# Kernel optimization log

Measured on AMD Instinct MI355X. Metric: run time of the kernel, lower is better.

Reference implementation:

```python
import jax, jax.numpy as jnp
import numpy as np

THRESH = 0.5
MARGIN = 0.1
SCALE_POS = 2.0
SCALE_NEG = 40.0
EPSILON = 1e-5


def setup_inputs() -> dict:
    key = jax.random.key(0)
    kx, kl = jax.random.split(key)
    B, D, N_CLASSES = 4096, 1024, 256
    x = jax.random.normal(kx, (B, D), dtype=jnp.float32)
    # L2-normalize embeddings (standard for multi-similarity loss; keeps sim in [-1, 1])
    x = x / jnp.linalg.norm(x, axis=1, keepdims=True)
    labels = jax.random.randint(kl, (B,), 0, N_CLASSES, dtype=jnp.int64)
    return {"x": x, "labels": labels}


def reference(x, labels):
    B = x.shape[0]
    sim = jnp.matmul(x, x.T)  # [B, B]

    eye = jnp.eye(B, dtype=bool)
    same = labels[:, None] == labels[None, :]
    pos_mask = same & ~eye                      # positives excl. self
    neg_mask = ~same                            # negatives
    pos_valid = pos_mask & (sim < 1.0 - EPSILON)  # pos_pair_ after < 1-eps filter

    # per-row hardest stats (inf/-inf where empty)
    min_pos = jnp.min(jnp.where(pos_valid, sim, jnp.inf), axis=1)   # min over pos_pair_
    max_neg = jnp.max(jnp.where(neg_mask, sim, -jnp.inf), axis=1)   # max over neg_pair_

    # mined pairs
    neg_keep = neg_mask & (sim + MARGIN > min_pos[:, None])
    pos_keep = pos_valid & (sim - MARGIN < max_neg[:, None])

    has_row = (pos_valid.any(axis=1) & neg_mask.any(axis=1)
               & pos_keep.any(axis=1) & neg_keep.any(axis=1))

    pos_sum = jnp.sum(jnp.where(pos_keep, jnp.exp(-SCALE_POS * (sim - THRESH)), 0.0), axis=1)
    neg_sum = jnp.sum(jnp.where(neg_keep, jnp.exp(SCALE_NEG * (sim - THRESH)), 0.0), axis=1)

    pos_loss = jnp.log1p(pos_sum) / SCALE_POS
    neg_loss = jnp.log1p(neg_sum) / SCALE_NEG

    row_loss = jnp.where(has_row, pos_loss + neg_loss, 0.0)
    return jnp.sum(row_loss) / B
```

## Files before the change

### kernel.cpp

```cpp
#include <hip/hip_runtime.h>
#include <hip/hip_bf16.h>
#include <math.h>
#include <stdint.h>


#define THRESH    0.5f
#define MARGIN    0.1f
#define SCALE_POS 2.0f
#define SCALE_NEG 40.0f
#define POS_CAP   (1.0f - 1e-5f)

typedef __bf16 bf16x8 __attribute__((ext_vector_type(8)));
typedef float  f32x4  __attribute__((ext_vector_type(4)));

__device__ __forceinline__ uint16_t f2bf(float f) {
  union { float f; uint32_t u; } v; v.f = f;
  uint32_t u = v.u;
  u += 0x7FFFu + ((u >> 16) & 1u);
  return (uint16_t)(u >> 16);
}

__global__ __launch_bounds__(256) void cvt_bf16_kernel(
    const float* __restrict__ x, uint16_t* __restrict__ y, int n) {
  int i = (blockIdx.x * 256 + threadIdx.x) * 4;
  if (i + 3 < n) {
    float4 v = *(const float4*)(x + i);
    ushort4 o;
    o.x = f2bf(v.x); o.y = f2bf(v.y); o.z = f2bf(v.z); o.w = f2bf(v.w);
    *(ushort4*)(y + i) = o;
  }
}

#if defined(__has_builtin)
#if __has_builtin(__builtin_amdgcn_global_load_lds)
#define HAVE_GLL 1
#endif
#endif

__device__ __forceinline__ void stage16(const uint16_t* g, uint16_t* lds_wave_base, int lane) {
#ifdef HAVE_GLL
  __builtin_amdgcn_global_load_lds(
      (const __attribute__((address_space(1))) void*)g,
      (__attribute__((address_space(3))) void*)lds_wave_base, 16, 0, 0);
#else
  *(uint4*)(lds_wave_base + lane * 8) = *(const uint4*)g;
#endif
}

__global__ __launch_bounds__(256) void simgemm_kernel(
    const uint16_t* __restrict__ X, float* __restrict__ C, int B, int D) {
  __shared__ __align__(16) uint16_t sA[128 * 32];
  __shared__ __align__(16) uint16_t sB[128 * 32];

  const int tid  = threadIdx.x;
  const int wave = tid >> 6;
  const int lane = tid & 63;
  const int waveM = wave >> 1, waveN = wave & 1;
  const int bm = blockIdx.x * 128;
  const int bn = blockIdx.y * 128;

  const int ch0 = tid;
  const int ch1 = tid + 256;
  const int r0 = ch0 >> 2, c0 = (ch0 & 3) * 8;
  const int r1 = ch1 >> 2, c1 = (ch1 & 3) * 8;

  const uint16_t* gA = X + (size_t)bm * D;
  const uint16_t* gB = X + (size_t)bn * D;

  uint16_t* lA0 = sA + wave * 512;
  uint16_t* lA1 = sA + 2048 + wave * 512;
  uint16_t* lB0 = sB + wave * 512;
  uint16_t* lB1 = sB + 2048 + wave * 512;

  const int fr = lane & 15;
  const int fq = lane >> 4;
  const int aoff = (waveM * 64 + fr) * 32 + fq * 8;
  const int boff = (waveN * 64 + fr) * 32 + fq * 8;

  f32x4 acc[4][4] = {};

  for (int k0 = 0; k0 < D; k0 += 32) {
    stage16(gA + (size_t)r0 * D + k0 + c0, lA0, lane);
    stage16(gA + (size_t)r1 * D + k0 + c1, lA1, lane);
    stage16(gB + (size_t)r0 * D + k0 + c0, lB0, lane);
    stage16(gB + (size_t)r1 * D + k0 + c1, lB1, lane);
    __syncthreads();

    bf16x8 af[4], bfv[4];
#pragma unroll
    for (int t = 0; t < 4; ++t) af[t]  = *(const bf16x8*)(sA + aoff + t * 512);
#pragma unroll
    for (int t = 0; t < 4; ++t) bfv[t] = *(const bf16x8*)(sB + boff + t * 512);

#pragma unroll
    for (int mt = 0; mt < 4; ++mt)
#pragma unroll
      for (int nt = 0; nt < 4; ++nt)
        acc[mt][nt] = __builtin_amdgcn_mfma_f32_16x16x32_bf16(
            af[mt], bfv[nt], acc[mt][nt], 0, 0, 0);
    __syncthreads();
  }

#pragma unroll
  for (int mt = 0; mt < 4; ++mt) {
#pragma unroll
    for (int nt = 0; nt < 4; ++nt) {
      const int col = bn + waveN * 64 + nt * 16 + fr;
#pragma unroll
      for (int r = 0; r < 4; ++r) {
        const int row = bm + waveM * 64 + mt * 16 + fq * 4 + r;
        C[(size_t)row * B + col] = acc[mt][nt][r];
      }
    }
  }
}

__global__ __launch_bounds__(256) void rowloss_kernel(
    const float* __restrict__ sim, const int* __restrict__ labels,
    float* __restrict__ rowbuf, int B) {
  __shared__ int   slab[4096];
  __shared__ float red[8];

  const int i    = blockIdx.x;
  const int tid  = threadIdx.x;
  const int wave = tid >> 6;
  const int lane = tid & 63;
  const float* row = sim + (size_t)i * B;

  for (int t = tid; t < (B >> 2); t += 256)
    ((int4*)slab)[t] = ((const int4*)labels)[t];
  __syncthreads();

  const int li = slab[i];

  float minpos = __builtin_inff();
  float maxneg = -__builtin_inff();

  const int iters = B >> 10;
  for (int it = 0; it < iters; ++it) {
    const int j = it * 1024 + tid * 4;
    float4 v = *(const float4*)(row + j);
    float s4[4] = {v.x, v.y, v.z, v.w};
#pragma unroll
    for (int q = 0; q < 4; ++q) {
      const int jj = j + q;
      const float s = s4[q];
      if (slab[jj] == li) {
        if (jj != i && s < POS_CAP) minpos = fminf(minpos, s);
      } else {
        maxneg = fmaxf(maxneg, s);
      }
    }
  }

#pragma unroll
  for (int m = 32; m > 0; m >>= 1) {
    minpos = fminf(minpos, __shfl_xor(minpos, m, 64));
    maxneg = fmaxf(maxneg, __shfl_xor(maxneg, m, 64));
  }
  if (lane == 0) { red[wave] = minpos; red[4 + wave] = maxneg; }
  __syncthreads();
  minpos = fminf(fminf(red[0], red[1]), fminf(red[2], red[3]));
  maxneg = fmaxf(fmaxf(red[4], red[5]), fmaxf(red[6], red[7]));
  __syncthreads();

  float psum = 0.f, nsum = 0.f;
  for (int it = 0; it < iters; ++it) {
    const int j = it * 1024 + tid * 4;
    float4 v = *(const float4*)(row + j);
    float s4[4] = {v.x, v.y, v.z, v.w};
#pragma unroll
    for (int q = 0; q < 4; ++q) {
      const int jj = j + q;
      const float s = s4[q];
      if (slab[jj] == li) {
        if (jj != i && s < POS_CAP && (s - MARGIN < maxneg))
          psum += __expf(-SCALE_POS * (s - THRESH));
      } else {
        if (s + MARGIN > minpos)
          nsum += __expf(SCALE_NEG * (s - THRESH));
      }
    }
  }

#pragma unroll
  for (int m = 32; m > 0; m >>= 1) {
    psum += __shfl_xor(psum, m, 64);
    nsum += __shfl_xor(nsum, m, 64);
  }
  if (lane == 0) { red[wave] = psum; red[4 + wave] = nsum; }
  __syncthreads();

  if (tid == 0) {
    psum = red[0] + red[1] + red[2] + red[3];
    nsum = red[4] + red[5] + red[6] + red[7];
    const bool has_row = (minpos != __builtin_inff()) &&
                         (maxneg != -__builtin_inff()) &&
                         (psum > 0.f) && (nsum > 0.f);
    rowbuf[i] = has_row
        ? (log1pf(psum) * (1.0f / SCALE_POS) + log1pf(nsum) * (1.0f / SCALE_NEG))
        : 0.f;
  }
}

__global__ __launch_bounds__(256) void finalreduce_kernel(
    const float* __restrict__ rowbuf, float* __restrict__ out, int B) {
  __shared__ float red[4];
  const int tid  = threadIdx.x;
  const int wave = tid >> 6;
  const int lane = tid & 63;

  float s = 0.f;
  for (int j = tid * 4; j < B; j += 1024) {
    float4 v = *(const float4*)(rowbuf + j);
    s += v.x + v.y + v.z + v.w;
  }
#pragma unroll
  for (int m = 32; m > 0; m >>= 1) s += __shfl_xor(s, m, 64);
  if (lane == 0) red[wave] = s;
  __syncthreads();
  if (tid == 0)
    out[0] = (red[0] + red[1] + red[2] + red[3]) * (1.0f / (float)B);
}

extern "C" void kernel_launch(void* const* d_in, const int* in_sizes, int n_in,
                              void* d_out, int out_size, void* d_ws, size_t ws_size,
                              hipStream_t stream) {
  const float* x      = (const float*)d_in[0];
  const int*   labels = (const int*)d_in[1];
  float*       out    = (float*)d_out;

  const int B = in_sizes[1];
  const int D = in_sizes[0] / B;

  uint16_t* xbf = (uint16_t*)d_ws;
  size_t xbytes = (((size_t)B * D * 2) + 255) & ~(size_t)255;
  float* sim = (float*)((char*)d_ws + xbytes);
  size_t simbytes = (size_t)B * B * 4;
  float* rowbuf = (float*)((char*)d_ws + xbytes + simbytes);

  const int n = B * D;
  cvt_bf16_kernel<<<n / 1024, 256, 0, stream>>>(x, xbf, n);

  dim3 grid(B / 128, B / 128);
  simgemm_kernel<<<grid, 256, 0, stream>>>(xbf, sim, B, D);

  rowloss_kernel<<<B, 256, 0, stream>>>(sim, labels, rowbuf, B);
  finalreduce_kernel<<<1, 256, 0, stream>>>(rowbuf, out, B);
}
```

Before: 143.4 us.

## Exploit sim symmetry in GEMM and cache row values in registers for rowloss

The GEMM now computes only upper-triangular 128x128 tiles, writes each result to both mirrored positions, and on diagonal tiles skips the B-tile load by reading from the A tile. The rowloss kernel handles 4 rows per block, keeps labels in registers instead of staging all of them in LDS, and caches each row's 16 values per thread so the second pass does not reread global memory. This roughly halves the MFMA work. The cost is strided transposed stores that coalesce poorly, plus extra barriers and register pressure in rowloss.

Measured after the change: 149.7 us. 1.04x slower.

```diff
diff --git a/kernel.cpp b/kernel.cpp
--- a/kernel.cpp
+++ b/kernel.cpp
@@ -49,6 +49,11 @@
 
 __global__ __launch_bounds__(256) void simgemm_kernel(
     const uint16_t* __restrict__ X, float* __restrict__ C, int B, int D) {
+  const int bi = blockIdx.x;
+  const int bj = blockIdx.y;
+  if (bj < bi) return;
+  const bool diag = (bi == bj);
+
   __shared__ __align__(16) uint16_t sA[128 * 32];
   __shared__ __align__(16) uint16_t sB[128 * 32];
 
@@ -56,8 +61,8 @@
   const int wave = tid >> 6;
   const int lane = tid & 63;
   const int waveM = wave >> 1, waveN = wave & 1;
-  const int bm = blockIdx.x * 128;
-  const int bn = blockIdx.y * 128;
+  const int bm = bi * 128;
+  const int bn = bj * 128;
 
   const int ch0 = tid;
   const int ch1 = tid + 256;
@@ -77,20 +82,24 @@
   const int aoff = (waveM * 64 + fr) * 32 + fq * 8;
   const int boff = (waveN * 64 + fr) * 32 + fq * 8;
 
+  const uint16_t* sBsrc = diag ? sA : sB;
+
   f32x4 acc[4][4] = {};
 
   for (int k0 = 0; k0 < D; k0 += 32) {
     stage16(gA + (size_t)r0 * D + k0 + c0, lA0, lane);
     stage16(gA + (size_t)r1 * D + k0 + c1, lA1, lane);
-    stage16(gB + (size_t)r0 * D + k0 + c0, lB0, lane);
-    stage16(gB + (size_t)r1 * D + k0 + c1, lB1, lane);
+    if (!diag) {
+      stage16(gB + (size_t)r0 * D + k0 + c0, lB0, lane);
+      stage16(gB + (size_t)r1 * D + k0 + c1, lB1, lane);
+    }
     __syncthreads();
 
     bf16x8 af[4], bfv[4];
 #pragma unroll
     for (int t = 0; t < 4; ++t) af[t]  = *(const bf16x8*)(sA + aoff + t * 512);
 #pragma unroll
-    for (int t = 0; t < 4; ++t) bfv[t] = *(const bf16x8*)(sB + boff + t * 512);
+    for (int t = 0; t < 4; ++t) bfv[t] = *(const bf16x8*)(sBsrc + boff + t * 512);
 
 #pragma unroll
     for (int mt = 0; mt < 4; ++mt)
@@ -110,6 +119,7 @@
       for (int r = 0; r < 4; ++r) {
         const int row = bm + waveM * 64 + mt * 16 + fq * 4 + r;
         C[(size_t)row * B + col] = acc[mt][nt][r];
+        if (!diag) C[(size_t)col * B + row] = acc[mt][nt][r];
       }
     }
   }
@@ -118,88 +128,97 @@
 __global__ __launch_bounds__(256) void rowloss_kernel(
     const float* __restrict__ sim, const int* __restrict__ labels,
     float* __restrict__ rowbuf, int B) {
-  __shared__ int   slab[4096];
   __shared__ float red[8];
 
-  const int i    = blockIdx.x;
+  const int base = blockIdx.x * 4;
   const int tid  = threadIdx.x;
   const int wave = tid >> 6;
   const int lane = tid & 63;
-  const float* row = sim + (size_t)i * B;
-
-  for (int t = tid; t < (B >> 2); t += 256)
-    ((int4*)slab)[t] = ((const int4*)labels)[t];
-  __syncthreads();
-
-  const int li = slab[i];
-
-  float minpos = __builtin_inff();
-  float maxneg = -__builtin_inff();
-
-  const int iters = B >> 10;
-  for (int it = 0; it < iters; ++it) {
-    const int j = it * 1024 + tid * 4;
-    float4 v = *(const float4*)(row + j);
-    float s4[4] = {v.x, v.y, v.z, v.w};
-#pragma unroll
-    for (int q = 0; q < 4; ++q) {
-      const int jj = j + q;
-      const float s = s4[q];
-      if (slab[jj] == li) {
-        if (jj != i && s < POS_CAP) minpos = fminf(minpos, s);
-      } else {
-        maxneg = fmaxf(maxneg, s);
+
+  int lab[16];
+#pragma unroll
+  for (int s = 0; s < 4; ++s) {
+    const int j = s * 1024 + tid * 4;
+    int4 lv = *(const int4*)(labels + j);
+    lab[s * 4 + 0] = lv.x; lab[s * 4 + 1] = lv.y;
+    lab[s * 4 + 2] = lv.z; lab[s * 4 + 3] = lv.w;
+  }
+
+  for (int r = 0; r < 4; ++r) {
+    const int i  = base + r;
+    const int li = labels[i];
+    const float* row = sim + (size_t)i * B;
+
+    float sv[16];
+    unsigned same = 0;
+    unsigned vpos = 0;
+    float minpos = __builtin_inff();
+    float maxneg = -__builtin_inff();
+
+#pragma unroll
+    for (int s = 0; s < 4; ++s) {
+      const int j = s * 1024 + tid * 4;
+      float4 v = *(const float4*)(row + j);
+      float s4[4] = {v.x, v.y, v.z, v.w};
+#pragma unroll
+      for (int q = 0; q < 4; ++q) {
+        const int idx = s * 4 + q;
+        const int jj  = j + q;
+        const float sij = s4[q];
+        sv[idx] = sij;
+        if (lab[idx] == li) {
+          same |= (1u << idx);
+          if (jj != i && sij < POS_CAP) {
+            vpos |= (1u << idx);
+            minpos = fminf(minpos, sij);
+          }
+        } else {
+          maxneg = fmaxf(maxneg, sij);
+        }
       }
     }
-  }
-
-#pragma unroll
-  for (int m = 32; m > 0; m >>= 1) {
-    minpos = fminf(minpos, __shfl_xor(minpos, m, 64));
-    maxneg = fmaxf(maxneg, __shfl_xor(maxneg, m, 64));
-  }
-  if (lane == 0) { red[wave] = minpos; red[4 + wave] = maxneg; }
-  __syncthreads();
-  minpos = fminf(fminf(red[0], red[1]), fminf(red[2], red[3]));
-  maxneg = fmaxf(fmaxf(red[4], red[5]), fmaxf(red[6], red[7]));
-  __syncthreads();
-
-  float psum = 0.f, nsum = 0.f;
-  for (int it = 0; it < iters; ++it) {
-    const int j = it * 1024 + tid * 4;
-    float4 v = *(const float4*)(row + j);
-    float s4[4] = {v.x, v.y, v.z, v.w};
-#pragma unroll
-    for (int q = 0; q < 4; ++q) {
-      const int jj = j + q;
-      const float s = s4[q];
-      if (slab[jj] == li) {
-        if (jj != i && s < POS_CAP && (s - MARGIN < maxneg))
-          psum += __expf(-SCALE_POS * (s - THRESH));
-      } else {
-        if (s + MARGIN > minpos)
-          nsum += __expf(SCALE_NEG * (s - THRESH));
+
+#pragma unroll
+    for (int m = 32; m > 0; m >>= 1) {
+      minpos = fminf(minpos, __shfl_xor(minpos, m, 64));
+      maxneg = fmaxf(maxneg, __shfl_xor(maxneg, m, 64));
+    }
+    if (lane == 0) { red[wave] = minpos; red[4 + wave] = maxneg; }
+    __syncthreads();
+    minpos = fminf(fminf(red[0], red[1]), fminf(red[2], red[3]));
+    maxneg = fmaxf(fmaxf(red[4], red[5]), fmaxf(red[6], red[7]));
+    __syncthreads();
+
+    float psum = 0.f, nsum = 0.f;
+#pragma unroll
+    for (int idx = 0; idx < 16; ++idx) {
+      const float sij = sv[idx];
+      if ((vpos >> idx) & 1u) {
+        if (sij - MARGIN < maxneg) psum += __expf(-SCALE_POS * (sij - THRESH));
+      } else if (!((same >> idx) & 1u)) {
+        if (sij + MARGIN > minpos) nsum += __expf(SCALE_NEG * (sij - THRESH));
       }
     }
-  }
-
-#pragma unroll
-  for (int m = 32; m > 0; m >>= 1) {
-    psum += __shfl_xor(psum, m, 64);
-    nsum += __shfl_xor(nsum, m, 64);
-  }
-  if (lane == 0) { red[wave] = psum; red[4 + wave] = nsum; }
-  __syncthreads();
-
-  if (tid == 0) {
-    psum = red[0] + red[1] + red[2] + red[3];
-    nsum = red[4] + red[5] + red[6] + red[7];
-    const bool has_row = (minpos != __builtin_inff()) &&
-                         (maxneg != -__builtin_inff()) &&
-                         (psum > 0.f) && (nsum > 0.f);
-    rowbuf[i] = has_row
-        ? (log1pf(psum) * (1.0f / SCALE_POS) + log1pf(nsum) * (1.0f / SCALE_NEG))
-        : 0.f;
+
+#pragma unroll
+    for (int m = 32; m > 0; m >>= 1) {
+      psum += __shfl_xor(psum, m, 64);
+      nsum += __shfl_xor(nsum, m, 64);
+    }
+    if (lane == 0) { red[wave] = psum; red[4 + wave] = nsum; }
+    __syncthreads();
+
+    if (tid == 0) {
+      psum = red[0] + red[1] + red[2] + red[3];
+      nsum = red[4] + red[5] + red[6] + red[7];
+      const bool has_row = (minpos != __builtin_inff()) &&
+                           (maxneg != -__builtin_inff()) &&
+                           (psum > 0.f) && (nsum > 0.f);
+      rowbuf[i] = has_row
+          ? (log1pf(psum) * (1.0f / SCALE_POS) + log1pf(nsum) * (1.0f / SCALE_NEG))
+          : 0.f;
+    }
+    __syncthreads();
   }
 }
 
@@ -245,6 +264,6 @@
   dim3 grid(B / 128, B / 128);
   simgemm_kernel<<<grid, 256, 0, stream>>>(xbf, sim, B, D);
 
-  rowloss_kernel<<<B, 256, 0, stream>>>(sim, labels, rowbuf, B);
+  rowloss_kernel<<<B / 4, 256, 0, stream>>>(sim, labels, rowbuf, B);
   finalreduce_kernel<<<1, 256, 0, stream>>>(rowbuf, out, B);
 }
```
